# Kernel tuning notes

Hardware: AMD Instinct MI355X
Metric: run time of the kernel (lower is better)

The kernel has to match this reference:

```python
import jax, jax.numpy as jnp
import numpy as np

B, S, D, H = 2, 2048, 1280, 16
DEPTH = D // H  # 80


def setup_inputs() -> dict:
    key = jax.random.key(0)
    ks = jax.random.split(key, 6)
    scale = 1.0 / np.sqrt(D)
    x = jax.random.normal(ks[0], (B, S, D), dtype=jnp.float32)
    # causal mask: 1.0 where attention is disallowed (strict upper triangle)
    mask = jnp.triu(jnp.ones((S, S), dtype=jnp.float32), k=1)
    Wq = jax.random.normal(ks[1], (D, D), dtype=jnp.float32) * scale
    Wk = jax.random.normal(ks[2], (D, D), dtype=jnp.float32) * scale
    Wv = jax.random.normal(ks[3], (D, D), dtype=jnp.float32) * scale
    Wo = jax.random.normal(ks[4], (D, D), dtype=jnp.float32) * scale
    z = jnp.zeros((D,), dtype=jnp.float32)
    return {"x": x, "mask": mask, "Wq": Wq, "bq": z, "Wk": Wk, "bk": z,
            "Wv": Wv, "bv": z, "Wo": Wo, "bo": z}


def _split_heads(t):
    # [B, S, D] -> [B, H, S, depth]
    return t.reshape(B, -1, H, DEPTH).transpose(0, 2, 1, 3)


def reference(x, mask, Wq, bq, Wk, bk, Wv, bv, Wo, bo):
    q = _split_heads(x @ Wq + bq)
    k = _split_heads(x @ Wk + bk)
    v = _split_heads(x @ Wv + bv)
    # scaled dot-product attention with additive (masked * -10000) logits
    logits = jnp.einsum("bhqd,bhkd->bhqk", q, k) / jnp.sqrt(
        jnp.asarray(DEPTH, dtype=jnp.float32))
    logits = logits + mask * -10000.0  # mask broadcasts over [B, H]
    attn = jax.nn.softmax(logits, axis=-1)
    ctx = jnp.einsum("bhqk,bhkd->bhqd", attn, v)
    ctx = ctx.transpose(0, 2, 1, 3).reshape(B, -1, D)  # merge heads
    return ctx @ Wo + bo
```

## Files before the change

kernel.cpp:

```cpp
#include <hip/hip_runtime.h>

typedef unsigned short u16;
typedef __bf16 bf16;
typedef __bf16 bf16x8 __attribute__((ext_vector_type(8)));
typedef unsigned short u16x8 __attribute__((ext_vector_type(8)));
typedef float f32x4 __attribute__((ext_vector_type(4)));

constexpr int B_ = 2, S_ = 2048, D_ = 1280, H_ = 16, DEPTH_ = 80;
constexpr int M_ = B_ * S_;
constexpr int QR_ = 128;

__device__ inline u16 f2b(float f) { return __builtin_bit_cast(u16, (bf16)f); }

typedef __attribute__((address_space(1))) const void gvoid;
typedef __attribute__((address_space(3))) void lvoid;
__device__ inline void gl_lds16(const void* g, void* l) {
  __builtin_amdgcn_global_load_lds((gvoid*)g, (lvoid*)l, 16, 0, 0);
}

__global__ __launch_bounds__(256) void prep_k(const float* __restrict__ x,
                                              u16* __restrict__ xbf,
                                              u16* __restrict__ QK,
                                              const float* __restrict__ W0,
                                              const float* __restrict__ W1,
                                              const float* __restrict__ W2,
                                              const float* __restrict__ W3,
                                              u16* __restrict__ WT) {
  __shared__ u16 t[32][33];
  int bid = blockIdx.x, tid = threadIdx.x;
  if (bid < 2560) {
    int i0 = (bid * 256 + tid) * 8;
    u16x8 v;
#pragma unroll
    for (int j = 0; j < 8; ++j) v[j] = f2b(x[i0 + j]);
    *(u16x8*)(xbf + i0) = v;
  } else if (bid < 5632) {
    int c = (bid - 2560) * 256 + tid;
    int r = c / 6, k = c - r * 6;
    u16x8 z = {};
    *(u16x8*)(QK + (size_t)r * QR_ + 80 + k * 8) = z;
  } else {
    int tt = bid - 5632;
    int z = tt / 1600, w = tt - z * 1600;
    int x0 = (w % 40) * 32, y0 = (w / 40) * 32;
    const float* srcs[4] = {W0, W1, W2, W3};
    const float* W = srcs[z];
    u16* out = WT + (size_t)z * D_ * D_;
    int tx = tid & 31, ty = tid >> 5;
#pragma unroll
    for (int i = 0; i < 4; ++i)
      t[ty + 8 * i][tx] = f2b(W[(size_t)(y0 + ty + 8 * i) * D_ + x0 + tx]);
    __syncthreads();
#pragma unroll
    for (int i = 0; i < 4; ++i)
      out[(size_t)(x0 + ty + 8 * i) * D_ + y0 + tx] = t[tx][ty + 8 * i];
  }
}

struct GemmAcc {
  f32x4 acc[4][4];
};
__device__ inline void gemm_core(const u16* __restrict__ A,
                                 const u16* __restrict__ BT, int m0, int n0,
                                 u16* a_s, u16* b_s, GemmAcc& g) {
  int tid = threadIdx.x, lane = tid & 63, wave = tid >> 6;
  int quad = lane >> 4, l15 = lane & 15;
  int wm = wave >> 1, wn = wave & 1;
  int r4 = lane >> 2, c4 = (lane & 3) * 8;

  for (int k0 = 0; k0 < D_; k0 += 32) {
    __syncthreads();
#pragma unroll
    for (int j = 0; j < 2; ++j) {
      int ch = wave * 2 + j;
      gl_lds16(A + (size_t)(m0 + ch * 16 + r4) * D_ + k0 + c4, a_s + ch * 512);
      gl_lds16(BT + (size_t)(n0 + ch * 16 + r4) * D_ + k0 + c4, b_s + ch * 512);
    }
    __syncthreads();
    bf16x8 af[4], bfr[4];
#pragma unroll
    for (int mt = 0; mt < 4; ++mt)
      af[mt] = *(const bf16x8*)(a_s + (wm * 64 + mt * 16 + l15) * 32 + quad * 8);
#pragma unroll
    for (int nt = 0; nt < 4; ++nt)
      bfr[nt] = *(const bf16x8*)(b_s + (wn * 64 + nt * 16 + l15) * 32 + quad * 8);
#pragma unroll
    for (int mt = 0; mt < 4; ++mt)
#pragma unroll
      for (int nt = 0; nt < 4; ++nt)
        g.acc[mt][nt] = __builtin_amdgcn_mfma_f32_16x16x32_bf16(
            af[mt], bfr[nt], g.acc[mt][nt], 0, 0, 0);
  }
}

__global__ __launch_bounds__(256, 4) void gemm_out(const u16* __restrict__ A,
                                                   const u16* __restrict__ BT,
                                                   const float* __restrict__ bias,
                                                   float* __restrict__ out) {
  __shared__ __align__(16) u16 a_s[128 * 32];
  __shared__ __align__(16) u16 b_s[128 * 32];
  int lane = threadIdx.x & 63, wave = threadIdx.x >> 6;
  int quad = lane >> 4, l15 = lane & 15;
  int wm = wave >> 1, wn = wave & 1;
  int m0 = blockIdx.y * 128, n0 = blockIdx.x * 128;

  GemmAcc g = {};
  gemm_core(A, BT, m0, n0, a_s, b_s, g);

#pragma unroll
  for (int nt = 0; nt < 4; ++nt) {
    int col = n0 + wn * 64 + nt * 16 + l15;
    float bv = bias[col];
#pragma unroll
    for (int mt = 0; mt < 4; ++mt)
#pragma unroll
      for (int r = 0; r < 4; ++r) {
        int row = m0 + wm * 64 + mt * 16 + quad * 4 + r;
        out[(size_t)row * D_ + col] = g.acc[mt][nt][r] + bv;
      }
  }
}

__device__ inline void stage_half(const u16* __restrict__ gsrc, int half,
                                  u16* lbase, int wave, int lane) {
  int rl = lane >> 3, c8 = lane & 7;
  int sc = (c8 ^ rl) << 3;
#pragma unroll
  for (int i = 0; i < 2; ++i) {
    int j = half * 16 + wave * 2 + i;
    gl_lds16(gsrc + (size_t)(j * 8 + rl) * D_ + sc, lbase + j * 512);
  }
}

__device__ inline bf16x8 frd(const u16* b, int r, int g) {
  return *(const bf16x8*)(b + r * 64 + ((g ^ (r & 7)) << 3));
}

__global__ __launch_bounds__(512, 2) void gemm_qkv8(
    const u16* __restrict__ A, const u16* __restrict__ BT,
    const float* __restrict__ bq, const float* __restrict__ bk,
    const float* __restrict__ bv, u16* __restrict__ Qw, u16* __restrict__ Kw,
    u16* __restrict__ Vw) {
  __shared__ __align__(16) u16 AS[2][256 * 64];
  __shared__ __align__(16) u16 BS[2][256 * 64];
  constexpr int BK = 64, NT = D_ / BK;
  int tid = threadIdx.x, lane = tid & 63, wave = tid >> 6;
  int quad = lane >> 4, l15 = lane & 15;
  int wm = wave >> 2, wn = wave & 3;
  int m0 = blockIdx.y * 256, n0 = blockIdx.x * 256;
  const u16* Ab = A + (size_t)m0 * D_;
  const u16* Bb = BT + (size_t)n0 * D_;

  f32x4 acc[8][4] = {};

  stage_half(Ab, 0, (u16*)AS[0], wave, lane);
  stage_half(Ab, 1, (u16*)AS[0], wave, lane);
  stage_half(Bb, 0, (u16*)BS[0], wave, lane);
  stage_half(Bb, 1, (u16*)BS[0], wave, lane);
  stage_half(Bb + BK, 0, (u16*)BS[1], wave, lane);
  stage_half(Bb + BK, 1, (u16*)BS[1], wave, lane);
  asm volatile("s_waitcnt vmcnt(4)" ::: "memory");
  __builtin_amdgcn_s_barrier();

  bf16x8 a[4][2], bl[2][2], bh[2][2];
  int ra = wm * 128 + l15, rb = wn * 64 + l15;

#pragma unroll 2
  for (int T = 0; T < NT; ++T) {
    const u16* Ac = AS[T & 1];
    const u16* Bc = BS[T & 1];
    u16* An = (u16*)AS[(T + 1) & 1];
    u16* Bcur = (u16*)BS[T & 1];

#pragma unroll
    for (int mt = 0; mt < 4; ++mt)
#pragma unroll
      for (int kh = 0; kh < 2; ++kh)
        a[mt][kh] = frd(Ac, ra + mt * 16, kh * 4 + quad);
#pragma unroll
    for (int nt = 0; nt < 2; ++nt)
#pragma unroll
      for (int kh = 0; kh < 2; ++kh)
        bl[nt][kh] = frd(Bc, rb + nt * 16, kh * 4 + quad);
    if (T + 1 < NT) stage_half(Ab + (size_t)(T + 1) * BK, 0, An, wave, lane);
    asm volatile("" ::: "memory");
    __builtin_amdgcn_s_barrier();
    __builtin_amdgcn_s_setprio(1);
#pragma unroll
    for (int mt = 0; mt < 4; ++mt)
#pragma unroll
      for (int nt = 0; nt < 2; ++nt)
#pragma unroll
        for (int kh = 0; kh < 2; ++kh)
          acc[mt][nt] = __builtin_amdgcn_mfma_f32_16x16x32_bf16(
              a[mt][kh], bl[nt][kh], acc[mt][nt], 0, 0, 0);
    __builtin_amdgcn_s_setprio(0);
    asm volatile("" ::: "memory");
    __builtin_amdgcn_s_barrier();

#pragma unroll
    for (int nt = 0; nt < 2; ++nt)
#pragma unroll
      for (int kh = 0; kh < 2; ++kh)
        bh[nt][kh] = frd(Bc, rb + 32 + nt * 16, kh * 4 + quad);
    if (T + 1 < NT) stage_half(Ab + (size_t)(T + 1) * BK, 1, An, wave, lane);
    asm volatile("" ::: "memory");
    __builtin_amdgcn_s_barrier();
    __builtin_amdgcn_s_setprio(1);
#pragma unroll
    for (int mt = 0; mt < 4; ++mt)
#pragma unroll
      for (int nt = 0; nt < 2; ++nt)
#pragma unroll
        for (int kh = 0; kh < 2; ++kh)
          acc[mt][nt + 2] = __builtin_amdgcn_mfma_f32_16x16x32_bf16(
              a[mt][kh], bh[nt][kh], acc[mt][nt + 2], 0, 0, 0);
    __builtin_amdgcn_s_setprio(0);
    asm volatile("" ::: "memory");
    __builtin_amdgcn_s_barrier();

#pragma unroll
    for (int mt = 0; mt < 4; ++mt)
#pragma unroll
      for (int kh = 0; kh < 2; ++kh)
        a[mt][kh] = frd(Ac, ra + 64 + mt * 16, kh * 4 + quad);
    if (T + 2 < NT) stage_half(Bb + (size_t)(T + 2) * BK, 0, Bcur, wave, lane);
    asm volatile("" ::: "memory");
    __builtin_amdgcn_s_barrier();
    __builtin_amdgcn_s_setprio(1);
#pragma unroll
    for (int mt = 0; mt < 4; ++mt)
#pragma unroll
      for (int nt = 0; nt < 2; ++nt)
#pragma unroll
        for (int kh = 0; kh < 2; ++kh)
          acc[mt + 4][nt + 2] = __builtin_amdgcn_mfma_f32_16x16x32_bf16(
              a[mt][kh], bh[nt][kh], acc[mt + 4][nt + 2], 0, 0, 0);
    __builtin_amdgcn_s_setprio(0);
    asm volatile("" ::: "memory");
    __builtin_amdgcn_s_barrier();

    if (T + 2 < NT) stage_half(Bb + (size_t)(T + 2) * BK, 1, Bcur, wave, lane);
    asm volatile("" ::: "memory");
    __builtin_amdgcn_s_barrier();
    __builtin_amdgcn_s_setprio(1);
#pragma unroll
    for (int mt = 0; mt < 4; ++mt)
#pragma unroll
      for (int nt = 0; nt < 2; ++nt)
#pragma unroll
        for (int kh = 0; kh < 2; ++kh)
          acc[mt + 4][nt] = __builtin_amdgcn_mfma_f32_16x16x32_bf16(
              a[mt][kh], bl[nt][kh], acc[mt + 4][nt], 0, 0, 0);
    __builtin_amdgcn_s_setprio(0);
    if (T < NT - 2)
      asm volatile("s_waitcnt vmcnt(4)" ::: "memory");
    else if (T == NT - 2)
      asm volatile("s_waitcnt vmcnt(0)" ::: "memory");
    asm volatile("" ::: "memory");
    __builtin_amdgcn_s_barrier();
  }

  int mat = n0 / D_;
  const float* bp = (mat == 0) ? bq : (mat == 1 ? bk : bv);
#pragma unroll
  for (int nt = 0; nt < 4; ++nt) {
    int ng = n0 + wn * 64 + nt * 16 + l15;
    int co = ng - mat * D_;
    float bb = bp[co];
    int h = co / DEPTH_, d = co % DEPTH_;
#pragma unroll
    for (int mt = 0; mt < 8; ++mt)
#pragma unroll
      for (int r = 0; r < 4; ++r) {
        int row = m0 + wm * 128 + mt * 16 + quad * 4 + r;
        int b = row >> 11, s = row & (S_ - 1);
        u16 bits = f2b(acc[mt][nt][r] + bb);
        if (mat < 2) {
          u16* outp = mat ? Kw : Qw;
          outp[((size_t)(b * H_ + h) * S_ + s) * QR_ + d] = bits;
        } else {
          Vw[((size_t)(b * H_ + h) * DEPTH_ + d) * S_ + s] = bits;
        }
      }
  }
}

__global__ __launch_bounds__(256, 4) void attn_k(const u16* __restrict__ Qp,
                                                 const u16* __restrict__ Kp,
                                                 const u16* __restrict__ VT,
                                                 u16* __restrict__ ctx) {
  constexpr float SCALE = 0.11180339887498949f;
  __shared__ __align__(16) u16 k_s[64 * 128];
  __shared__ __align__(16) u16 vt_s[80 * 64];
  __shared__ __align__(16) u16 p_s[64 * 72];
  int tid = threadIdx.x, lane = tid & 63, wave = tid >> 6;
  int quad = lane >> 4, l15 = lane & 15;
  int bx = blockIdx.x, by = blockIdx.y;
  int s_ = (by >> 4) & 1;
  int qt = s_ ? (31 - bx) : bx;
  int bh = (by & 15) | (((by >> 5) & 1) << 4);
  const u16* Qb = Qp + (size_t)bh * S_ * QR_;
  const u16* Kb = Kp + (size_t)bh * S_ * QR_;
  const u16* Vb = VT + (size_t)bh * DEPTH_ * S_;

  bf16x8 qf[3];
#pragma unroll
  for (int ks = 0; ks < 3; ++ks)
    qf[ks] = *(const bf16x8*)(Qb + (size_t)(qt * 64 + wave * 16 + l15) * QR_ +
                              ks * 32 + quad * 8);

  f32x4 acc_o[5] = {};
  float lsum[4] = {};

  for (int kt = 0; kt <= qt; ++kt) {
    int k0 = kt * 64;
    __syncthreads();
#pragma unroll
    for (int i = 0; i < 4; ++i) {
      int row = wave * 4 + quad + 16 * i;
      int sc = l15 ^ (row & 7);
      gl_lds16(Kb + (size_t)(k0 + row) * QR_ + sc * 8,
               k_s + (size_t)row * QR_ + l15 * 8);
    }
#pragma unroll
    for (int i = 0; i < 3; ++i) {
      int ch = tid + 256 * i;
      if (ch < 640) {
        int row = ch >> 3, pos = ch & 7;
        int sc = pos ^ (row & 7);
        gl_lds16(Vb + (size_t)row * S_ + k0 + sc * 8, vt_s + ch * 8);
      }
    }
    __syncthreads();

    f32x4 sa[4] = {};
#pragma unroll
    for (int ks = 0; ks < 3; ++ks) {
      int pa = ((ks * 4 + quad) ^ (l15 & 7)) * 8;
#pragma unroll
      for (int nt = 0; nt < 4; ++nt) {
        bf16x8 bfr = *(const bf16x8*)(k_s + (size_t)(nt * 16 + l15) * QR_ + pa);
        sa[nt] = __builtin_amdgcn_mfma_f32_16x16x32_bf16(qf[ks], bfr, sa[nt], 0, 0, 0);
      }
    }
    bool diag = (kt == qt);
#pragma unroll
    for (int nt = 0; nt < 4; ++nt)
#pragma unroll
      for (int r = 0; r < 4; ++r) {
        float p = __expf(sa[nt][r] * SCALE);
        if (diag && (nt * 16 + l15) > (wave * 16 + quad * 4 + r)) p = 0.0f;
        sa[nt][r] = p;
        lsum[r] += p;
      }
    asm volatile("s_waitcnt lgkmcnt(0)" ::: "memory");
#pragma unroll
    for (int nt = 0; nt < 4; ++nt)
#pragma unroll
      for (int r = 0; r < 4; ++r)
        p_s[(wave * 16 + quad * 4 + r) * 72 + nt * 16 + l15] = f2b(sa[nt][r]);
    asm volatile("s_waitcnt lgkmcnt(0)" ::: "memory");
#pragma unroll
    for (int kk = 0; kk < 2; ++kk) {
      bf16x8 af = *(const bf16x8*)(p_s + (wave * 16 + l15) * 72 + kk * 32 + quad * 8);
#pragma unroll
      for (int d5 = 0; d5 < 5; ++d5) {
        int pv = ((kk * 4 + quad) ^ (l15 & 7)) * 8;
        bf16x8 bfr = *(const bf16x8*)(vt_s + (size_t)(d5 * 16 + l15) * 64 + pv);
        acc_o[d5] = __builtin_amdgcn_mfma_f32_16x16x32_bf16(af, bfr, acc_o[d5], 0, 0, 0);
      }
    }
  }

#pragma unroll
  for (int r = 0; r < 4; ++r)
#pragma unroll
    for (int m = 1; m < 16; m <<= 1) lsum[r] += __shfl_xor(lsum[r], m, 16);

  int b = bh >> 4, h = bh & 15;
#pragma unroll
  for (int d5 = 0; d5 < 5; ++d5)
#pragma unroll
    for (int r = 0; r < 4; ++r) {
      int s = qt * 64 + wave * 16 + quad * 4 + r;
      int col = h * DEPTH_ + d5 * 16 + l15;
      ctx[(size_t)(b * S_ + s) * D_ + col] = f2b(acc_o[d5][r] / lsum[r]);
    }
}

extern "C" void kernel_launch(void* const* d_in, const int* in_sizes, int n_in,
                              void* d_out, int out_size, void* d_ws, size_t ws_size,
                              hipStream_t stream) {
  const float* x  = (const float*)d_in[0];
  const float* Wq = (const float*)d_in[2];
  const float* bq = (const float*)d_in[3];
  const float* Wk = (const float*)d_in[4];
  const float* bk = (const float*)d_in[5];
  const float* Wv = (const float*)d_in[6];
  const float* bv = (const float*)d_in[7];
  const float* Wo = (const float*)d_in[8];
  const float* bo = (const float*)d_in[9];

  const size_t DD = (size_t)D_ * D_;
  const size_t QE = (size_t)B_ * H_ * S_ * DEPTH_;
  const size_t QP = (size_t)B_ * H_ * S_ * QR_;
  u16* xbf = (u16*)d_ws;
  u16* wT  = xbf + QE;
  u16* Qw  = wT + 4 * DD;
  u16* Kw  = Qw + QP;
  u16* Vw  = Kw + QP;
  u16* Cw  = xbf;
  size_t need = (size_t)(Vw + QE - xbf) * 2;
  if (ws_size < need) return;

  prep_k<<<12032, 256, 0, stream>>>(x, xbf, Qw, Wq, Wk, Wv, Wo, wT);
  gemm_qkv8<<<dim3(3 * D_ / 256, M_ / 256), 512, 0, stream>>>(xbf, wT, bq, bk, bv,
                                                              Qw, Kw, Vw);
  attn_k<<<dim3(16, 64), 256, 0, stream>>>(Qw, Kw, Vw, Cw);
  gemm_out<<<dim3(D_ / 128, M_ / 128), 256, 0, stream>>>(Cw, wT + 3 * DD, bo,
                                                         (float*)d_out);
}
```

Measured before the change: 272.0 us.

## Enlarge attention query tiles to 128 rows, swizzle QKV GEMM blocks, vectorize V stores

The attention kernel now uses 512 threads (8 waves) per block and covers 128 query rows against 64-key tiles. Each K/V tile staged in LDS is therefore reused by twice as many queries, roughly halving K/V global traffic, at the cost of fewer, larger blocks and a coarser causal load balance. The QKV GEMM moves to a 1D grid with a block-index swizzle meant to improve cache locality across dies. Its V-transpose epilogue now writes four consecutive bf16 values with one vector store instead of four scalar stores.

Result: no change. 271.5 us (-0.2%).

```diff
diff --git a/kernel.cpp b/kernel.cpp
--- a/kernel.cpp
+++ b/kernel.cpp
@@ -4,6 +4,7 @@
 typedef __bf16 bf16;
 typedef __bf16 bf16x8 __attribute__((ext_vector_type(8)));
 typedef unsigned short u16x8 __attribute__((ext_vector_type(8)));
+typedef unsigned short u16x4 __attribute__((ext_vector_type(4)));
 typedef float f32x4 __attribute__((ext_vector_type(4)));
 
 constexpr int B_ = 2, S_ = 2048, D_ = 1280, H_ = 16, DEPTH_ = 80;
@@ -147,7 +148,10 @@
   int tid = threadIdx.x, lane = tid & 63, wave = tid >> 6;
   int quad = lane >> 4, l15 = lane & 15;
   int wm = wave >> 2, wn = wave & 3;
-  int m0 = blockIdx.y * 256, n0 = blockIdx.x * 256;
+  int bid = blockIdx.x;
+  int sw = (bid & 7) * 30 + (bid >> 3);
+  int by = sw / 15, bx = sw - by * 15;
+  int m0 = by * 256, n0 = bx * 256;
   const u16* Ab = A + (size_t)m0 * D_;
   const u16* Bb = BT + (size_t)n0 * D_;
 
@@ -262,43 +266,56 @@
   }
 
   int mat = n0 / D_;
-  const float* bp = (mat == 0) ? bq : (mat == 1 ? bk : bv);
-#pragma unroll
-  for (int nt = 0; nt < 4; ++nt) {
-    int ng = n0 + wn * 64 + nt * 16 + l15;
-    int co = ng - mat * D_;
-    float bb = bp[co];
-    int h = co / DEPTH_, d = co % DEPTH_;
-#pragma unroll
-    for (int mt = 0; mt < 8; ++mt)
-#pragma unroll
-      for (int r = 0; r < 4; ++r) {
-        int row = m0 + wm * 128 + mt * 16 + quad * 4 + r;
+  if (mat == 2) {
+#pragma unroll
+    for (int nt = 0; nt < 4; ++nt) {
+      int co = n0 + wn * 64 + nt * 16 + l15 - 2 * D_;
+      float bb_ = bv[co];
+      int h = co / DEPTH_, d = co % DEPTH_;
+#pragma unroll
+      for (int mt = 0; mt < 8; ++mt) {
+        int row = m0 + wm * 128 + mt * 16 + quad * 4;
         int b = row >> 11, s = row & (S_ - 1);
-        u16 bits = f2b(acc[mt][nt][r] + bb);
-        if (mat < 2) {
-          u16* outp = mat ? Kw : Qw;
-          outp[((size_t)(b * H_ + h) * S_ + s) * QR_ + d] = bits;
-        } else {
-          Vw[((size_t)(b * H_ + h) * DEPTH_ + d) * S_ + s] = bits;
+        u16x4 pk;
+#pragma unroll
+        for (int r = 0; r < 4; ++r) pk[r] = f2b(acc[mt][nt][r] + bb_);
+        *(u16x4*)(Vw + ((size_t)(b * H_ + h) * DEPTH_ + d) * S_ + s) = pk;
+      }
+    }
+  } else {
+    const float* bp = (mat == 0) ? bq : bk;
+    u16* outp = mat ? Kw : Qw;
+#pragma unroll
+    for (int nt = 0; nt < 4; ++nt) {
+      int co = n0 + wn * 64 + nt * 16 + l15 - mat * D_;
+      float bb_ = bp[co];
+      int h = co / DEPTH_, d = co % DEPTH_;
+#pragma unroll
+      for (int mt = 0; mt < 8; ++mt)
+#pragma unroll
+        for (int r = 0; r < 4; ++r) {
+          int row = m0 + wm * 128 + mt * 16 + quad * 4 + r;
+          int b = row >> 11, s = row & (S_ - 1);
+          outp[((size_t)(b * H_ + h) * S_ + s) * QR_ + d] =
+              f2b(acc[mt][nt][r] + bb_);
         }
-      }
-  }
-}
-
-__global__ __launch_bounds__(256, 4) void attn_k(const u16* __restrict__ Qp,
+    }
+  }
+}
+
+__global__ __launch_bounds__(512, 4) void attn_k(const u16* __restrict__ Qp,
                                                  const u16* __restrict__ Kp,
                                                  const u16* __restrict__ VT,
                                                  u16* __restrict__ ctx) {
   constexpr float SCALE = 0.11180339887498949f;
   __shared__ __align__(16) u16 k_s[64 * 128];
   __shared__ __align__(16) u16 vt_s[80 * 64];
-  __shared__ __align__(16) u16 p_s[64 * 72];
+  __shared__ __align__(16) u16 p_s[128 * 72];
   int tid = threadIdx.x, lane = tid & 63, wave = tid >> 6;
   int quad = lane >> 4, l15 = lane & 15;
   int bx = blockIdx.x, by = blockIdx.y;
   int s_ = (by >> 4) & 1;
-  int qt = s_ ? (31 - bx) : bx;
+  int qt = s_ ? bx : (15 - bx);
   int bh = (by & 15) | (((by >> 5) & 1) << 4);
   const u16* Qb = Qp + (size_t)bh * S_ * QR_;
   const u16* Kb = Kp + (size_t)bh * S_ * QR_;
@@ -307,26 +324,28 @@
   bf16x8 qf[3];
 #pragma unroll
   for (int ks = 0; ks < 3; ++ks)
-    qf[ks] = *(const bf16x8*)(Qb + (size_t)(qt * 64 + wave * 16 + l15) * QR_ +
+    qf[ks] = *(const bf16x8*)(Qb + (size_t)(qt * 128 + wave * 16 + l15) * QR_ +
                               ks * 32 + quad * 8);
 
   f32x4 acc_o[5] = {};
   float lsum[4] = {};
-
-  for (int kt = 0; kt <= qt; ++kt) {
+  int nkt = 2 * qt + 2;
+
+  for (int kt = 0; kt < nkt; ++kt) {
     int k0 = kt * 64;
     __syncthreads();
 #pragma unroll
-    for (int i = 0; i < 4; ++i) {
-      int row = wave * 4 + quad + 16 * i;
+    for (int i = 0; i < 2; ++i) {
+      int row = (wave * 2 + i) * 4 + quad;
       int sc = l15 ^ (row & 7);
       gl_lds16(Kb + (size_t)(k0 + row) * QR_ + sc * 8,
                k_s + (size_t)row * QR_ + l15 * 8);
     }
 #pragma unroll
-    for (int i = 0; i < 3; ++i) {
-      int ch = tid + 256 * i;
-      if (ch < 640) {
+    for (int i = 0; i < 2; ++i) {
+      int j = wave + 8 * i;
+      if (j < 10) {
+        int ch = j * 64 + lane;
         int row = ch >> 3, pos = ch & 7;
         int sc = pos ^ (row & 7);
         gl_lds16(Vb + (size_t)row * S_ + k0 + sc * 8, vt_s + ch * 8);
@@ -344,13 +363,15 @@
         sa[nt] = __builtin_amdgcn_mfma_f32_16x16x32_bf16(qf[ks], bfr, sa[nt], 0, 0, 0);
       }
     }
-    bool diag = (kt == qt);
+    bool diag = (kt >= 2 * qt);
 #pragma unroll
     for (int nt = 0; nt < 4; ++nt)
 #pragma unroll
       for (int r = 0; r < 4; ++r) {
         float p = __expf(sa[nt][r] * SCALE);
-        if (diag && (nt * 16 + l15) > (wave * 16 + quad * 4 + r)) p = 0.0f;
+        if (diag &&
+            (k0 + nt * 16 + l15) > (qt * 128 + wave * 16 + quad * 4 + r))
+          p = 0.0f;
         sa[nt][r] = p;
         lsum[r] += p;
       }
@@ -383,7 +404,7 @@
   for (int d5 = 0; d5 < 5; ++d5)
 #pragma unroll
     for (int r = 0; r < 4; ++r) {
-      int s = qt * 64 + wave * 16 + quad * 4 + r;
+      int s = qt * 128 + wave * 16 + quad * 4 + r;
       int col = h * DEPTH_ + d5 * 16 + l15;
       ctx[(size_t)(b * S_ + s) * D_ + col] = f2b(acc_o[d5][r] / lsum[r]);
     }
@@ -415,9 +436,8 @@
   if (ws_size < need) return;
 
   prep_k<<<12032, 256, 0, stream>>>(x, xbf, Qw, Wq, Wk, Wv, Wo, wT);
-  gemm_qkv8<<<dim3(3 * D_ / 256, M_ / 256), 512, 0, stream>>>(xbf, wT, bq, bk, bv,
-                                                              Qw, Kw, Vw);
-  attn_k<<<dim3(16, 64), 256, 0, stream>>>(Qw, Kw, Vw, Cw);
+  gemm_qkv8<<<240, 512, 0, stream>>>(xbf, wT, bq, bk, bv, Qw, Kw, Vw);
+  attn_k<<<dim3(8, 64), 512, 0, stream>>>(Qw, Kw, Vw, Cw);
   gemm_out<<<dim3(D_ / 128, M_ / 128), 256, 0, stream>>>(Cw, wT + 3 * DD, bo,
                                                          (float*)d_out);
 }
```
